# Kernel optimization log

Measured on AMD Instinct MI355X. Metric: run time of the kernel, lower is better.

The kernel has to match this reference:

```python
import jax, jax.numpy as jnp
import numpy as np

W_LEN = 37  # window_length
EPS = 1e-9
LRELU_SLOPE = 0.2
SQRT2 = 1.4142135623730951


def win_sum(x, w):
    # Depthwise sliding-window sum of width w, 'same' padding w//2 (odd w).
    # Equivalent to the diag-kernel conv1d in the original code, but O(T) via cumsum.
    pad = w // 2
    xp = jnp.pad(x, ((0, 0), (0, 0), (pad, pad)))
    cs = jnp.cumsum(xp, axis=-1)
    cs = jnp.pad(cs, ((0, 0), (0, 0), (1, 0)))
    return cs[..., w:] - cs[..., :-w]


def conv1d(x, w, b):
    # x: [B,C,T], w: [O,I,3], padding=1
    y = jax.lax.conv_general_dilated(x, w, (1,), [(1, 1)],
                                     dimension_numbers=('NCH', 'OIH', 'NCH'))
    return y + b[None, :, None]


def adawin_instance(x, s, mask, fc_w, fc_b, alpha):
    # x: [B,C,T], s: [B,S,T], mask: [B,T]
    C = x.shape[1]
    h = jnp.einsum('bst,cs->bct', s, fc_w) + fc_b[None, :, None]  # [B,2C,T]
    m = mask[:, None, :]                       # [B,1,T]
    denom = win_sum(m, W_LEN) + EPS            # same for all channels
    gamma = win_sum(h[:, :C], W_LEN) / denom * m
    beta = win_sum(h[:, C:], W_LEN) / denom * m
    x_norm = jnp.tanh(alpha * x)               # WindowedNorm1d.forward
    return (1.0 + gamma) * x_norm + beta


def setup_inputs() -> dict:
    key = jax.random.key(0)
    ks = jax.random.split(key, 10)
    B, C_IN, C_OUT, S, T = 16, 512, 512, 128, 2048
    inp = {
        'x': jax.random.normal(ks[0], (B, C_IN, T), dtype=jnp.float32),
        's': jax.random.normal(ks[1], (B, S, T), dtype=jnp.float32),
        'lengths': jax.random.randint(ks[2], (B,), 0, T).astype(jnp.int32),
        'fc1_w': jax.random.normal(ks[3], (2 * C_IN, S), dtype=jnp.float32) * 0.05,
        'fc1_b': jnp.zeros((2 * C_IN,), dtype=jnp.float32),
        'alpha1': jnp.full((1,), 0.5, dtype=jnp.float32),
        'conv1_w': jax.random.normal(ks[4], (C_OUT, C_IN, 3), dtype=jnp.float32) * 0.02,
        'conv1_b': jnp.zeros((C_OUT,), dtype=jnp.float32),
        'fc2_w': jax.random.normal(ks[5], (2 * C_OUT, S), dtype=jnp.float32) * 0.05,
        'fc2_b': jnp.zeros((2 * C_OUT,), dtype=jnp.float32),
        'alpha2': jnp.full((1,), 0.5, dtype=jnp.float32),
        'conv2_w': jax.random.normal(ks[6], (C_OUT, C_OUT, 3), dtype=jnp.float32) * 0.02,
        'conv2_b': jnp.zeros((C_OUT,), dtype=jnp.float32),
    }
    return inp


def reference(x, s, lengths, fc1_w, fc1_b, alpha1, conv1_w, conv1_b,
              fc2_w, fc2_b, alpha2, conv2_w, conv2_b):
    T = x.shape[2]
    mask = (jnp.arange(T)[None, :] < lengths[:, None]).astype(x.dtype)  # [B,T]

    h = adawin_instance(x, s, mask, fc1_w, fc1_b, alpha1)
    h = jax.nn.leaky_relu(h, LRELU_SLOPE)
    h = conv1d(h, conv1_w, conv1_b)
    h = adawin_instance(h, s, mask, fc2_w, fc2_b, alpha2)
    h = jax.nn.leaky_relu(h, LRELU_SLOPE)
    h = conv1d(h, conv2_w, conv2_b)

    # dim_in == dim_out -> identity shortcut
    return (h + x) / SQRT2
```

## Files before the change

### kernel.cpp

```cpp
#include <hip/hip_runtime.h>

#define B_ 16
#define C_ 512
#define S_ 128
#define T_ 2048
#define HALF 18
#define WLEN 37

typedef __bf16 bf16x8 __attribute__((ext_vector_type(8)));
typedef float f32x4 __attribute__((ext_vector_type(4)));
typedef float f32x16 __attribute__((ext_vector_type(16)));
typedef unsigned short ushort_t;

__device__ inline ushort_t f2bf(float x) {
    unsigned u = __float_as_uint(x);
    u += 0x7fffu + ((u >> 16) & 1u);
    return (ushort_t)(u >> 16);
}
__device__ inline float bf2f(ushort_t h) {
    return __uint_as_float(((unsigned)h) << 16);
}
__device__ inline float fast_tanh(float z) {
    float e = __expf(2.f * z);
    return 1.f - __fdividef(2.f, e + 1.f);
}
__device__ __forceinline__ void glds16(const void* g, void* l) {
    __builtin_amdgcn_global_load_lds(
        (const __attribute__((address_space(1))) unsigned*)g,
        (__attribute__((address_space(3))) unsigned*)l, 16, 0, 0);
}

#define MFMA16(a, b, c) __builtin_amdgcn_mfma_f32_16x16x32_bf16((a), (b), (c), 0, 0, 0)
#define MFMA32(a, b, c) __builtin_amdgcn_mfma_f32_32x32x16_bf16((a), (b), (c), 0, 0, 0)

__global__ void prep_weights(const float* __restrict__ fc1, const float* __restrict__ fc2,
                             ushort_t* __restrict__ Wfc) {
    const int n_fc = 1024 * 128;
    int idx = blockIdx.x * blockDim.x + threadIdx.x;
    if (idx < n_fc) Wfc[idx] = f2bf(fc1[idx]);
    else if (idx < 2 * n_fc) Wfc[idx] = f2bf(fc2[idx - n_fc]);
}

__global__ void prep_conv_images(const float* __restrict__ c1, const float* __restrict__ c2,
                                 ushort_t* __restrict__ I1, ushort_t* __restrict__ I2) {
    int idx = blockIdx.x * blockDim.x + threadIdx.x;
    const int per_conv = 4 * 16 * 1664;
    if (idx >= 2 * per_conv) return;
    int conv = idx >= per_conv;
    int rr = conv ? idx - per_conv : idx;
    const float* src = conv ? c2 : c1;
    ushort_t* dst = conv ? I2 : I1;
    int blkch = rr / 1664;
    int G = rr - blkch * 1664;
    int r = G / 13;
    int g = G - r * 13;
    ushort_t vals[8];
    if (g == 12) {
#pragma unroll
        for (int e = 0; e < 8; ++e) vals[e] = 0;
    } else {
        int tap = g >> 2, seg = g & 3;
        int o = (blkch >> 4) * 128 + r;
        int chb = (blkch & 15) * 32 + seg * 8;
#pragma unroll
        for (int e = 0; e < 8; ++e)
            vals[e] = f2bf(src[(size_t)(o * 512 + chb + e) * 3 + tap]);
    }
    uint4 pk;
    pk.x = vals[0] | ((unsigned)vals[1] << 16);
    pk.y = vals[2] | ((unsigned)vals[3] << 16);
    pk.z = vals[4] | ((unsigned)vals[5] << 16);
    pk.w = vals[6] | ((unsigned)vals[7] << 16);
    *(uint4*)&dst[(size_t)rr * 8] = pk;
}

__global__ void zero_pads(ushort_t* __restrict__ y1p, ushort_t* __restrict__ y2p) {
    int tid = blockIdx.x * blockDim.x + threadIdx.x;
    if (tid < 4096) {
        ushort_t* base = (tid & 1) ? y2p : y1p;
        int r = tid >> 1;
        int bb = r >> 7;
        int rowsel = (r >> 6) & 1;
        int col = (r & 63) * 8;
        size_t row = (size_t)bb * (T_ + 2) + (rowsel ? (T_ + 1) : 0);
        *(uint4*)&base[row * C_ + col] = (uint4){0, 0, 0, 0};
    }
}

__global__ __launch_bounds__(256) void winsum_kernel(const float* __restrict__ s,
                                                     ushort_t* __restrict__ sw_t) {
    int b = blockIdx.y;
    int t0 = blockIdx.x * 64;
    __shared__ float sb[128][101];
    int tid = threadIdx.x;
    for (int e = tid; e < 128 * 100; e += 256) {
        int sj = e / 100;
        int u = e - sj * 100;
        int gt = t0 - HALF + u;
        float v = 0.f;
        if (gt >= 0 && gt < T_) v = s[((size_t)(b * S_ + sj)) * T_ + gt];
        sb[sj][u] = v;
    }
    __syncthreads();
    for (int e = tid; e < 64 * 128; e += 256) {
        int tl = e >> 7;
        int sj = e & 127;
        float sum = 0.f;
#pragma unroll
        for (int d = 0; d < WLEN; ++d) sum += sb[sj][tl + d];
        sw_t[((size_t)(b * T_ + t0 + tl)) * S_ + sj] = f2bf(sum);
    }
}

template <int INLAYOUT>
__global__ __launch_bounds__(256) void adawin_kernel(
    const void* __restrict__ xin_, const ushort_t* __restrict__ sw_t,
    const ushort_t* __restrict__ Wfc, const float* __restrict__ fcb,
    const float* __restrict__ alpha, const int* __restrict__ lengths,
    ushort_t* __restrict__ youtp) {
    int t0 = blockIdx.x * 64;
    int c0 = blockIdx.y * 64;
    int b = blockIdx.z;
    __shared__ __attribute__((aligned(16))) ushort_t smem[128 * 136 + 64 * 136];
    ushort_t (*As)[136] = (ushort_t(*)[136])smem;
    ushort_t (*Bs)[136] = (ushort_t(*)[136])(smem + 128 * 136);
    int tid = threadIdx.x;

    {
        int r = tid >> 4;
        int cseg = (tid & 15) * 8;
#pragma unroll
        for (int p = 0; p < 8; ++p) {
            int row = p * 16 + r;
            int grow = (row < 64) ? (c0 + row) : (448 + c0 + row);
            *(uint4*)&As[row][cseg] = *(const uint4*)&Wfc[(size_t)grow * 128 + cseg];
        }
    }
    {
        int tl = tid & 63;
        int sg = tid >> 6;
        const ushort_t* src = &sw_t[((size_t)(b * T_ + t0 + tl)) * S_];
#pragma unroll
        for (int j = 0; j < 4; ++j) {
            int col = sg * 32 + j * 8;
            *(uint4*)&Bs[tl][col] = *(const uint4*)&src[col];
        }
    }
    __syncthreads();

    int wave = tid >> 6, lane = tid & 63;
    int quad = lane >> 4, l = lane & 15;
    f32x4 accg[4], accb[4];
#pragma unroll
    for (int n = 0; n < 4; ++n) {
        accg[n] = (f32x4){0.f, 0.f, 0.f, 0.f};
        accb[n] = (f32x4){0.f, 0.f, 0.f, 0.f};
    }
    int rg = wave * 16 + l;
    int rb = 64 + wave * 16 + l;
#pragma unroll
    for (int ks = 0; ks < 4; ++ks) {
        int kc = ks * 32 + quad * 8;
        bf16x8 ag = *(const bf16x8*)&As[rg][kc];
        bf16x8 ab = *(const bf16x8*)&As[rb][kc];
#pragma unroll
        for (int n = 0; n < 4; ++n) {
            bf16x8 bb = *(const bf16x8*)&Bs[n * 16 + l][kc];
            accg[n] = MFMA16(ag, bb, accg[n]);
            accb[n] = MFMA16(ab, bb, accb[n]);
        }
    }

    __syncthreads();
    ushort_t (*Ts)[72] = (ushort_t(*)[72])smem;

    int len = lengths[b];
    float alph = alpha[0];
    const float* xf = (const float*)xin_;
    const ushort_t* xh = (const ushort_t*)xin_;
    int clocal = wave * 16 + quad * 4;
    int cbase = c0 + clocal;
#pragma unroll
    for (int n = 0; n < 4; ++n) {
        int t = t0 + n * 16 + l;
        int lo = t - HALF; if (lo < 0) lo = 0;
        int hi = t + HALF; if (hi > T_ - 1) hi = T_ - 1;
        float cnt = (float)(hi - lo + 1);
        int hv = hi < (len - 1) ? hi : (len - 1);
        int mdi = hv - lo + 1; if (mdi < 0) mdi = 0;
        float m = (t < len) ? 1.f : 0.f;
        float sc = m / ((float)mdi + 1e-9f);

        float xv[4];
        if (INLAYOUT == 0) {
#pragma unroll
            for (int j = 0; j < 4; ++j)
                xv[j] = xf[(size_t)(b * C_ + cbase + j) * T_ + t];
        } else {
            uint2 xraw = *(const uint2*)&xh[((size_t)(b * (T_ + 2) + 1 + t)) * C_ + cbase];
            xv[0] = bf2f((ushort_t)(xraw.x & 0xffff));
            xv[1] = bf2f((ushort_t)(xraw.x >> 16));
            xv[2] = bf2f((ushort_t)(xraw.y & 0xffff));
            xv[3] = bf2f((ushort_t)(xraw.y >> 16));
        }
        unsigned pk[2];
#pragma unroll
        for (int j = 0; j < 4; ++j) {
            int c = cbase + j;
            float gamma = (accg[n][j] + fcb[c] * cnt) * sc;
            float beta = (accb[n][j] + fcb[C_ + c] * cnt) * sc;
            float xn = fast_tanh(alph * xv[j]);
            float v = (1.f + gamma) * xn + beta;
            v = v > 0.f ? v : 0.2f * v;
            unsigned hv16 = (unsigned)f2bf(v);
            if (j & 1) pk[j >> 1] |= hv16 << 16;
            else pk[j >> 1] = hv16;
        }
        *(uint2*)&Ts[n * 16 + l][clocal] = (uint2){pk[0], pk[1]};
    }
    __syncthreads();
    {
        int row = tid >> 2;
        int seg = (tid & 3) * 16;
        size_t gbase = ((size_t)(b * (T_ + 2) + 1 + t0 + row)) * C_ + c0 + seg;
        *(uint4*)&youtp[gbase] = *(const uint4*)&Ts[row][seg];
        *(uint4*)&youtp[gbase + 8] = *(const uint4*)&Ts[row][seg + 8];
    }
}

#define A_BYTES 26624
#define B_BYTES 11264
__device__ __forceinline__ void conv_stage(const char* aimg, const char* xt, int ch,
                                           char* Ab, char* Bb, int wave, int lane) {
#pragma unroll
    for (int i = 0; i < 37; ++i) {
        if ((i & 3) != wave) continue;
        if (i < 26) {
            glds16(aimg + i * 1024 + lane * 16, Ab + i * 1024);
        } else {
            int j = i - 26;
            int gi = j * 64 + lane;
            int r = gi / 5;
            int gg = gi - r * 5;
            if (gg == 4) gg = 0;
            glds16(xt + (size_t)r * 1024 + ch * 64 + gg * 16, Bb + j * 1024);
        }
    }
}

template <int EPI>
__global__ __launch_bounds__(256) void conv_kernel(
    const ushort_t* __restrict__ Xp, const ushort_t* __restrict__ Wimg,
    const float* __restrict__ bias, const float* __restrict__ resid,
    ushort_t* __restrict__ out_bf, float* __restrict__ out_f) {
    int t0 = blockIdx.x * 128;
    int o0 = blockIdx.y * 128;
    int b = blockIdx.z;
    __shared__ __attribute__((aligned(16))) char smembuf[2 * A_BYTES + 2 * B_BYTES];
    int tid = threadIdx.x;
    int lane = tid & 63, wave = tid >> 6;
    int l32 = lane & 31, khalf = lane >> 5;
    int wo = (wave & 1) * 64, wt = (wave >> 1) * 64;

    const char* imgbase = (const char*)Wimg + (size_t)blockIdx.y * 16 * A_BYTES;
    const char* xt = (const char*)Xp + (size_t)(b * (T_ + 2) + t0) * 1024;

    f32x16 acc[2][2];
#pragma unroll
    for (int io = 0; io < 2; ++io)
#pragma unroll
        for (int it = 0; it < 2; ++it)
#pragma unroll
            for (int r = 0; r < 16; ++r) acc[io][it][r] = 0.f;

    conv_stage(imgbase, xt, 0, smembuf, smembuf + 2 * A_BYTES, wave, lane);

#pragma unroll 1
    for (int ch = 0; ch < 16; ++ch) {
        int cur = ch & 1;
        if (ch < 15) {
            conv_stage(imgbase + (size_t)(ch + 1) * A_BYTES, xt, ch + 1,
                       smembuf + (cur ^ 1) * A_BYTES,
                       smembuf + 2 * A_BYTES + (cur ^ 1) * B_BYTES, wave, lane);
            if (wave == 0) asm volatile("s_waitcnt vmcnt(10)\ns_barrier" ::: "memory");
            else           asm volatile("s_waitcnt vmcnt(9)\ns_barrier" ::: "memory");
        } else {
            asm volatile("s_waitcnt vmcnt(0)\ns_barrier" ::: "memory");
        }
        ushort_t (*As)[104] = (ushort_t(*)[104])(smembuf + cur * A_BYTES);
        ushort_t (*Bs)[40] = (ushort_t(*)[40])(smembuf + 2 * A_BYTES + cur * B_BYTES);
#pragma unroll
        for (int tap = 0; tap < 3; ++tap) {
#pragma unroll
            for (int ks = 0; ks < 2; ++ks) {
                int kc = tap * 32 + ks * 16 + khalf * 8;
                bf16x8 a0 = *(const bf16x8*)&As[wo + l32][kc];
                bf16x8 a1 = *(const bf16x8*)&As[wo + 32 + l32][kc];
#pragma unroll
                for (int it = 0; it < 2; ++it) {
                    bf16x8 bb =
                        *(const bf16x8*)&Bs[wt + it * 32 + l32 + tap][ks * 16 + khalf * 8];
                    acc[0][it] = MFMA32(a0, bb, acc[0][it]);
                    acc[1][it] = MFMA32(a1, bb, acc[1][it]);
                }
            }
        }
        asm volatile("s_barrier" ::: "memory");
    }

    if (EPI == 0) {
        ushort_t (*Ts)[136] = (ushort_t(*)[136])smembuf;
#pragma unroll
        for (int io = 0; io < 2; ++io)
#pragma unroll
            for (int it = 0; it < 2; ++it) {
                int trow = wt + it * 32 + l32;
#pragma unroll
                for (int g = 0; g < 4; ++g) {
                    int oc = wo + io * 32 + g * 8 + khalf * 4;
                    unsigned pk[2];
#pragma unroll
                    for (int j = 0; j < 4; ++j) {
                        float v = acc[io][it][g * 4 + j] + bias[o0 + oc + j];
                        unsigned hv16 = (unsigned)f2bf(v);
                        if (j & 1) pk[j >> 1] |= hv16 << 16;
                        else pk[j >> 1] = hv16;
                    }
                    *(uint2*)&Ts[trow][oc] = (uint2){pk[0], pk[1]};
                }
            }
        __syncthreads();
        int cc = (tid & 15) * 8;
        int rbse = tid >> 4;
#pragma unroll
        for (int j = 0; j < 8; ++j) {
            int row = j * 16 + rbse;
            *(uint4*)&out_bf[((size_t)(b * (T_ + 2) + 1 + t0 + row)) * C_ + o0 + cc] =
                *(const uint4*)&Ts[row][cc];
        }
    } else {
#pragma unroll
        for (int io = 0; io < 2; ++io)
#pragma unroll
            for (int it = 0; it < 2; ++it) {
                int obase = o0 + wo + io * 32;
                int t = t0 + wt + it * 32 + l32;
#pragma unroll
                for (int g = 0; g < 4; ++g) {
                    int oo = obase + g * 8 + khalf * 4;
#pragma unroll
                    for (int j = 0; j < 4; ++j) {
                        size_t off = (size_t)(b * C_ + oo + j) * T_ + t;
                        out_f[off] = (acc[io][it][g * 4 + j] + bias[oo + j] + resid[off]) *
                                     0.70710678118654752f;
                    }
                }
            }
    }
}

extern "C" void kernel_launch(void* const* d_in, const int* in_sizes, int n_in,
                              void* d_out, int out_size, void* d_ws, size_t ws_size,
                              hipStream_t stream) {
    const float* x = (const float*)d_in[0];
    const float* s = (const float*)d_in[1];
    const int* lengths = (const int*)d_in[2];
    const float* fc1_w = (const float*)d_in[3];
    const float* fc1_b = (const float*)d_in[4];
    const float* alpha1 = (const float*)d_in[5];
    const float* conv1_w = (const float*)d_in[6];
    const float* conv1_b = (const float*)d_in[7];
    const float* fc2_w = (const float*)d_in[8];
    const float* fc2_b = (const float*)d_in[9];
    const float* alpha2 = (const float*)d_in[10];
    const float* conv2_w = (const float*)d_in[11];
    const float* conv2_b = (const float*)d_in[12];

    const size_t IMG = (size_t)4 * 16 * 1664 * 8;
    char* ws = (char*)d_ws;
    ushort_t* sw_t = (ushort_t*)ws; ws += (size_t)B_ * T_ * S_ * 2;
    ushort_t* Wfc = (ushort_t*)ws;  ws += (size_t)2 * 1024 * 128 * 2;
    ushort_t* I1 = (ushort_t*)ws;   ws += IMG * 2;
    ushort_t* I2 = (ushort_t*)ws;   ws += IMG * 2;
    ushort_t* y2p = (ushort_t*)ws;  ws += (size_t)B_ * (T_ + 2) * C_ * 2;
    ushort_t* y1p = (ushort_t*)ws;  ws += (size_t)B_ * (T_ + 2) * C_ * 2;
    ws += 12 * 1024;
    if ((size_t)(ws - (char*)d_ws) > ws_size) return;

    prep_weights<<<dim3(1024), dim3(256), 0, stream>>>(fc1_w, fc2_w, Wfc);
    prep_conv_images<<<dim3(832), dim3(256), 0, stream>>>(conv1_w, conv2_w, I1, I2);
    winsum_kernel<<<dim3(32, 16), dim3(256), 0, stream>>>(s, sw_t);
    zero_pads<<<dim3(16), dim3(256), 0, stream>>>(y1p, y2p);
    adawin_kernel<0><<<dim3(32, 8, 16), dim3(256), 0, stream>>>(
        (const void*)x, sw_t, Wfc, fc1_b, alpha1, lengths, y1p);
    conv_kernel<0><<<dim3(16, 4, 16), dim3(256), 0, stream>>>(
        y1p, I1, conv1_b, (const float*)nullptr, y2p, (float*)nullptr);
    adawin_kernel<1><<<dim3(32, 8, 16), dim3(256), 0, stream>>>(
        (const void*)y2p, sw_t, Wfc + 1024 * 128, fc2_b, alpha2, lengths, y1p);
    conv_kernel<1><<<dim3(16, 4, 16), dim3(256), 0, stream>>>(
        y1p, I2, conv2_b, x, (ushort_t*)nullptr, (float*)d_out);
}
```

Measured before the change: 359.2 us.

## Retile conv GEMM to 256x256 blocks with 8 waves and interleaved prefetch

The conv kernel moves from 128x128 output tiles on 4 waves to 256x256 tiles on 8 waves, so each block reuses A and B operands across a larger area. The weight image layout in prep_conv_images changes to match. Global-to-LDS prefetch for the next channel chunk is now split across the three tap phases and interleaved with MFMA issue, with s_setprio raised during MFMAs. LDS grows to about 150KB, so only one block fits per CU, and the grid shrinks to 256 blocks. That reduces occupancy and latency hiding in exchange for higher arithmetic intensity.

```diff
diff --git a/kernel.cpp b/kernel.cpp
--- a/kernel.cpp
+++ b/kernel.cpp
@@ -41,27 +41,31 @@
     else if (idx < 2 * n_fc) Wfc[idx] = f2bf(fc2[idx - n_fc]);
 }
 
+#define IMGCH 53248
+#define A_BYTES 53248
+#define B_BYTES 22528
 __global__ void prep_conv_images(const float* __restrict__ c1, const float* __restrict__ c2,
                                  ushort_t* __restrict__ I1, ushort_t* __restrict__ I2) {
     int idx = blockIdx.x * blockDim.x + threadIdx.x;
-    const int per_conv = 4 * 16 * 1664;
+    const int per_conv = 2 * 16 * 256 * 13;
     if (idx >= 2 * per_conv) return;
     int conv = idx >= per_conv;
     int rr = conv ? idx - per_conv : idx;
     const float* src = conv ? c2 : c1;
     ushort_t* dst = conv ? I2 : I1;
-    int blkch = rr / 1664;
-    int G = rr - blkch * 1664;
-    int r = G / 13;
-    int g = G - r * 13;
+    int imgchunk = rr / 3328;
+    int rem = rr - imgchunk * 3328;
+    int r = rem / 13;
+    int g = rem - r * 13;
+    int mb = imgchunk >> 4, ch = imgchunk & 15;
     ushort_t vals[8];
     if (g == 12) {
 #pragma unroll
         for (int e = 0; e < 8; ++e) vals[e] = 0;
     } else {
         int tap = g >> 2, seg = g & 3;
-        int o = (blkch >> 4) * 128 + r;
-        int chb = (blkch & 15) * 32 + seg * 8;
+        int o = mb * 256 + r;
+        int chb = ch * 32 + seg * 8;
 #pragma unroll
         for (int e = 0; e < 8; ++e)
             vals[e] = f2bf(src[(size_t)(o * 512 + chb + e) * 3 + tap]);
@@ -228,100 +232,138 @@
     }
 }
 
-#define A_BYTES 26624
-#define B_BYTES 11264
-__device__ __forceinline__ void conv_stage(const char* aimg, const char* xt, int ch,
-                                           char* Ab, char* Bb, int wave, int lane) {
-#pragma unroll
-    for (int i = 0; i < 37; ++i) {
-        if ((i & 3) != wave) continue;
-        if (i < 26) {
-            glds16(aimg + i * 1024 + lane * 16, Ab + i * 1024);
-        } else {
-            int j = i - 26;
-            int gi = j * 64 + lane;
-            int r = gi / 5;
-            int gg = gi - r * 5;
-            if (gg == 4) gg = 0;
-            glds16(xt + (size_t)r * 1024 + ch * 64 + gg * 16, Bb + j * 1024);
-        }
+__device__ __forceinline__ void issue_g(int g, const char* img, const char* xt, int ch,
+                                        char* Ab, char* Bb, int lane) {
+    if (g < 52) {
+        glds16(img + g * 1024 + lane * 16, Ab + g * 1024);
+    } else if (g < 74) {
+        int j = g - 52;
+        int gi = j * 64 + lane;
+        int r = gi / 5;
+        int gg = gi - r * 5;
+        if (gg == 4) gg = 0;
+        if (r > 257) r = 257;
+        glds16(xt + (size_t)r * 1024 + ch * 64 + gg * 16, Bb + j * 1024);
+    } else {
+        int j = g - 74;
+        glds16(img + j * 1024 + lane * 16, Ab + j * 1024);
+    }
+}
+template <int G0, int G1>
+__device__ __forceinline__ void issue_batch(const char* img, const char* xt, int ch,
+                                            char* Ab, char* Bb, int wave, int lane) {
+#pragma unroll
+    for (int g = G0; g < G1; ++g) {
+        if ((g & 7) != wave) continue;
+        issue_g(g, img, xt, ch, Ab, Bb, lane);
     }
 }
 
 template <int EPI>
-__global__ __launch_bounds__(256) void conv_kernel(
+__global__ __launch_bounds__(512, 2) void conv_kernel(
     const ushort_t* __restrict__ Xp, const ushort_t* __restrict__ Wimg,
     const float* __restrict__ bias, const float* __restrict__ resid,
     ushort_t* __restrict__ out_bf, float* __restrict__ out_f) {
-    int t0 = blockIdx.x * 128;
-    int o0 = blockIdx.y * 128;
+    int t0 = blockIdx.x * 256;
+    int o0 = blockIdx.y * 256;
     int b = blockIdx.z;
-    __shared__ __attribute__((aligned(16))) char smembuf[2 * A_BYTES + 2 * B_BYTES];
+    __shared__ __attribute__((aligned(16))) char smem[2 * A_BYTES + 2 * B_BYTES];
     int tid = threadIdx.x;
     int lane = tid & 63, wave = tid >> 6;
     int l32 = lane & 31, khalf = lane >> 5;
-    int wo = (wave & 1) * 64, wt = (wave >> 1) * 64;
-
-    const char* imgbase = (const char*)Wimg + (size_t)blockIdx.y * 16 * A_BYTES;
+    int wm = wave >> 2, wn = wave & 3;
+
+    const char* imgch = (const char*)Wimg + (size_t)blockIdx.y * 16 * IMGCH;
     const char* xt = (const char*)Xp + (size_t)(b * (T_ + 2) + t0) * 1024;
 
-    f32x16 acc[2][2];
-#pragma unroll
-    for (int io = 0; io < 2; ++io)
-#pragma unroll
-        for (int it = 0; it < 2; ++it)
-#pragma unroll
-            for (int r = 0; r < 16; ++r) acc[io][it][r] = 0.f;
-
-    conv_stage(imgbase, xt, 0, smembuf, smembuf + 2 * A_BYTES, wave, lane);
+    f32x16 acc[4][2];
+#pragma unroll
+    for (int m = 0; m < 4; ++m)
+#pragma unroll
+        for (int nf = 0; nf < 2; ++nf)
+#pragma unroll
+            for (int r = 0; r < 16; ++r) acc[m][nf][r] = 0.f;
+
+    char* A0 = smem;
+    char* A1 = smem + A_BYTES;
+    char* Bb0 = smem + 2 * A_BYTES;
+    char* Bb1 = Bb0 + B_BYTES;
+
+    issue_batch<0, 80>(imgch, xt, 0, A0, Bb0, wave, lane);
+    issue_batch<0, 32>(imgch + IMGCH, xt, 1, A1, Bb1, wave, lane);
+    asm volatile("s_waitcnt vmcnt(4)" ::: "memory");
+    asm volatile("s_barrier" ::: "memory");
 
 #pragma unroll 1
     for (int ch = 0; ch < 16; ++ch) {
         int cur = ch & 1;
-        if (ch < 15) {
-            conv_stage(imgbase + (size_t)(ch + 1) * A_BYTES, xt, ch + 1,
-                       smembuf + (cur ^ 1) * A_BYTES,
-                       smembuf + 2 * A_BYTES + (cur ^ 1) * B_BYTES, wave, lane);
-            if (wave == 0) asm volatile("s_waitcnt vmcnt(10)\ns_barrier" ::: "memory");
-            else           asm volatile("s_waitcnt vmcnt(9)\ns_barrier" ::: "memory");
-        } else {
-            asm volatile("s_waitcnt vmcnt(0)\ns_barrier" ::: "memory");
-        }
-        ushort_t (*As)[104] = (ushort_t(*)[104])(smembuf + cur * A_BYTES);
-        ushort_t (*Bs)[40] = (ushort_t(*)[40])(smembuf + 2 * A_BYTES + cur * B_BYTES);
-#pragma unroll
-        for (int tap = 0; tap < 3; ++tap) {
-#pragma unroll
-            for (int ks = 0; ks < 2; ++ks) {
-                int kc = tap * 32 + ks * 16 + khalf * 8;
-                bf16x8 a0 = *(const bf16x8*)&As[wo + l32][kc];
-                bf16x8 a1 = *(const bf16x8*)&As[wo + 32 + l32][kc];
-#pragma unroll
-                for (int it = 0; it < 2; ++it) {
-                    bf16x8 bb =
-                        *(const bf16x8*)&Bs[wt + it * 32 + l32 + tap][ks * 16 + khalf * 8];
-                    acc[0][it] = MFMA32(a0, bb, acc[0][it]);
-                    acc[1][it] = MFMA32(a1, bb, acc[1][it]);
-                }
+        char* Ac = smem + cur * A_BYTES;
+        char* Bc = smem + 2 * A_BYTES + cur * B_BYTES;
+        char* An = smem + (cur ^ 1) * A_BYTES;
+        char* Bn = smem + 2 * A_BYTES + (cur ^ 1) * B_BYTES;
+        ushort_t (*As)[104] = (ushort_t(*)[104])Ac;
+        ushort_t (*Bs)[40] = (ushort_t(*)[40])Bc;
+        const char* img_n1 = imgch + (size_t)(ch + 1) * IMGCH;
+
+#pragma unroll
+        for (int p = 0; p < 3; ++p) {
+            bf16x8 af[2][4], bf[2][2];
+#pragma unroll
+            for (int m = 0; m < 4; ++m) {
+                const ushort_t* ar = &As[wm * 128 + m * 32 + l32][p * 32 + khalf * 8];
+                af[0][m] = *(const bf16x8*)ar;
+                af[1][m] = *(const bf16x8*)(ar + 16);
             }
-        }
-        asm volatile("s_barrier" ::: "memory");
+#pragma unroll
+            for (int nf = 0; nf < 2; ++nf) {
+                const ushort_t* br = &Bs[wn * 64 + nf * 32 + l32 + p][khalf * 8];
+                bf[0][nf] = *(const bf16x8*)br;
+                bf[1][nf] = *(const bf16x8*)(br + 16);
+            }
+            if (ch < 15) {
+                if (p == 0) issue_batch<32, 56>(img_n1, xt, ch + 1, An, Bn, wave, lane);
+                else if (p == 1) issue_batch<56, 80>(img_n1, xt, ch + 1, An, Bn, wave, lane);
+            }
+            asm volatile("s_barrier" ::: "memory");
+            asm volatile("s_waitcnt lgkmcnt(0)" ::: "memory");
+            __builtin_amdgcn_sched_barrier(0);
+            __builtin_amdgcn_s_setprio(1);
+#pragma unroll
+            for (int ks = 0; ks < 2; ++ks)
+#pragma unroll
+                for (int m = 0; m < 4; ++m)
+#pragma unroll
+                    for (int nf = 0; nf < 2; ++nf)
+                        acc[m][nf] = MFMA32(af[ks][m], bf[ks][nf], acc[m][nf]);
+            __builtin_amdgcn_s_setprio(0);
+            asm volatile("s_barrier" ::: "memory");
+        }
+        if (ch < 14) {
+            issue_batch<0, 32>(imgch + (size_t)(ch + 2) * IMGCH, xt, ch + 2, Ac, Bc,
+                               wave, lane);
+            asm volatile("s_waitcnt vmcnt(4)" ::: "memory");
+            asm volatile("s_barrier" ::: "memory");
+        } else if (ch == 14) {
+            asm volatile("s_waitcnt vmcnt(0)" ::: "memory");
+            asm volatile("s_barrier" ::: "memory");
+        }
     }
 
     if (EPI == 0) {
-        ushort_t (*Ts)[136] = (ushort_t(*)[136])smembuf;
-#pragma unroll
-        for (int io = 0; io < 2; ++io)
-#pragma unroll
-            for (int it = 0; it < 2; ++it) {
-                int trow = wt + it * 32 + l32;
+        __syncthreads();
+        ushort_t (*Ts)[264] = (ushort_t(*)[264])smem;
+#pragma unroll
+        for (int nf = 0; nf < 2; ++nf) {
+            int trow = wn * 64 + nf * 32 + l32;
+#pragma unroll
+            for (int m = 0; m < 4; ++m) {
 #pragma unroll
                 for (int g = 0; g < 4; ++g) {
-                    int oc = wo + io * 32 + g * 8 + khalf * 4;
+                    int oc = wm * 128 + m * 32 + g * 8 + khalf * 4;
                     unsigned pk[2];
 #pragma unroll
                     for (int j = 0; j < 4; ++j) {
-                        float v = acc[io][it][g * 4 + j] + bias[o0 + oc + j];
+                        float v = acc[m][nf][g * 4 + j] + bias[o0 + oc + j];
                         unsigned hv16 = (unsigned)f2bf(v);
                         if (j & 1) pk[j >> 1] |= hv16 << 16;
                         else pk[j >> 1] = hv16;
@@ -329,29 +371,27 @@
                     *(uint2*)&Ts[trow][oc] = (uint2){pk[0], pk[1]};
                 }
             }
+        }
         __syncthreads();
-        int cc = (tid & 15) * 8;
-        int rbse = tid >> 4;
-#pragma unroll
-        for (int j = 0; j < 8; ++j) {
-            int row = j * 16 + rbse;
-            *(uint4*)&out_bf[((size_t)(b * (T_ + 2) + 1 + t0 + row)) * C_ + o0 + cc] =
-                *(const uint4*)&Ts[row][cc];
-        }
+        int row = tid >> 1;
+        int colh = (tid & 1) * 128;
+        size_t gbase = ((size_t)(b * (T_ + 2) + 1 + t0 + row)) * C_ + o0 + colh;
+#pragma unroll
+        for (int j = 0; j < 16; ++j)
+            *(uint4*)&out_bf[gbase + j * 8] = *(const uint4*)&Ts[row][colh + j * 8];
     } else {
 #pragma unroll
-        for (int io = 0; io < 2; ++io)
-#pragma unroll
-            for (int it = 0; it < 2; ++it) {
-                int obase = o0 + wo + io * 32;
-                int t = t0 + wt + it * 32 + l32;
+        for (int m = 0; m < 4; ++m)
+#pragma unroll
+            for (int nf = 0; nf < 2; ++nf) {
+                int t = t0 + wn * 64 + nf * 32 + l32;
 #pragma unroll
                 for (int g = 0; g < 4; ++g) {
-                    int oo = obase + g * 8 + khalf * 4;
+                    int oo = o0 + wm * 128 + m * 32 + g * 8 + khalf * 4;
 #pragma unroll
                     for (int j = 0; j < 4; ++j) {
                         size_t off = (size_t)(b * C_ + oo + j) * T_ + t;
-                        out_f[off] = (acc[io][it][g * 4 + j] + bias[oo + j] + resid[off]) *
+                        out_f[off] = (acc[m][nf][g * 4 + j] + bias[oo + j] + resid[off]) *
                                      0.70710678118654752f;
                     }
                 }
@@ -376,12 +416,12 @@
     const float* conv2_w = (const float*)d_in[11];
     const float* conv2_b = (const float*)d_in[12];
 
-    const size_t IMG = (size_t)4 * 16 * 1664 * 8;
+    const size_t IMGB = (size_t)2 * 16 * IMGCH;
     char* ws = (char*)d_ws;
     ushort_t* sw_t = (ushort_t*)ws; ws += (size_t)B_ * T_ * S_ * 2;
     ushort_t* Wfc = (ushort_t*)ws;  ws += (size_t)2 * 1024 * 128 * 2;
-    ushort_t* I1 = (ushort_t*)ws;   ws += IMG * 2;
-    ushort_t* I2 = (ushort_t*)ws;   ws += IMG * 2;
+    ushort_t* I1 = (ushort_t*)ws;   ws += IMGB;
+    ushort_t* I2 = (ushort_t*)ws;   ws += IMGB;
     ushort_t* y2p = (ushort_t*)ws;  ws += (size_t)B_ * (T_ + 2) * C_ * 2;
     ushort_t* y1p = (ushort_t*)ws;  ws += (size_t)B_ * (T_ + 2) * C_ * 2;
     ws += 12 * 1024;
@@ -393,10 +433,10 @@
     zero_pads<<<dim3(16), dim3(256), 0, stream>>>(y1p, y2p);
     adawin_kernel<0><<<dim3(32, 8, 16), dim3(256), 0, stream>>>(
         (const void*)x, sw_t, Wfc, fc1_b, alpha1, lengths, y1p);
-    conv_kernel<0><<<dim3(16, 4, 16), dim3(256), 0, stream>>>(
+    conv_kernel<0><<<dim3(8, 2, 16), dim3(512), 0, stream>>>(
         y1p, I1, conv1_b, (const float*)nullptr, y2p, (float*)nullptr);
     adawin_kernel<1><<<dim3(32, 8, 16), dim3(256), 0, stream>>>(
         (const void*)y2p, sw_t, Wfc + 1024 * 128, fc2_b, alpha2, lengths, y1p);
-    conv_kernel<1><<<dim3(16, 4, 16), dim3(256), 0, stream>>>(
+    conv_kernel<1><<<dim3(8, 2, 16), dim3(512), 0, stream>>>(
         y1p, I2, conv2_b, x, (ushort_t*)nullptr, (float*)d_out);
 }
```

Result: slower. 371.0 us (+3.3%).
